# Optimization experiments

Measured on AMD Instinct MI355X. Metric: run time of the kernel, lower is better.

Reference implementation:

```python
import jax, jax.numpy as jnp
import numpy as np

N = 50000      # nodes
E = 640000     # edges
HID = 64       # hid_dim (per-head channels C)
HEADS = 4
D = HID * HEADS  # 256, conv output dim (concat=True)
LN_EPS = 1e-5


def setup_inputs() -> dict:
    key = jax.random.key(0)
    ks = jax.random.split(key, 10)
    def w(k, shape, scale=0.05):
        return jax.random.normal(k, shape, dtype=jnp.float32) * scale
    x = jax.random.normal(ks[0], (N, HID), dtype=jnp.float32)
    edge_index = jax.random.randint(ks[1], (2, E), 0, N)
    return {
        'x': x,
        'edge_index': edge_index,
        'Wq': w(ks[2], (D, HID)), 'bq': jnp.zeros((D,), jnp.float32),
        'Wk': w(ks[3], (D, HID)), 'bk': jnp.zeros((D,), jnp.float32),
        'Wv': w(ks[4], (D, HID)), 'bv': jnp.zeros((D,), jnp.float32),
        'Wskip': w(ks[5], (D, HID)), 'bskip': jnp.zeros((D,), jnp.float32),
        'Wbeta': w(ks[6], (1, 3 * D)),
        'ln_g': jnp.ones((D,), jnp.float32), 'ln_b': jnp.zeros((D,), jnp.float32),
        'Wproj': w(ks[7], (HID, D)), 'bproj': jnp.zeros((HID,), jnp.float32),
    }


def _layer(x, edge_index, Wq, bq, Wk, bk, Wv, bv, Wskip, bskip, Wbeta, ln_g, ln_b, Wproj, bproj):
    src, dst = edge_index[0], edge_index[1]  # message flows src -> dst
    # q/k/v projections, [N, H, C]
    q = (x @ Wq.T + bq).reshape(N, HEADS, HID)
    k = (x @ Wk.T + bk).reshape(N, HEADS, HID)
    v = (x @ Wv.T + bv).reshape(N, HEADS, HID)
    # edge-wise attention logits: [E, H]
    alpha = jnp.einsum('ehc,ehc->eh', q[dst], k[src]) / jnp.sqrt(jnp.float32(HID))
    # per-destination-node softmax (segment softmax)
    m = jax.ops.segment_max(alpha, dst, num_segments=N)          # [N, H]
    ex = jnp.exp(alpha - m[dst])                                 # [E, H]
    s = jax.ops.segment_sum(ex, dst, num_segments=N)             # [N, H]
    attn = ex / (s[dst] + 1e-16)                                 # [E, H]
    # weighted scatter-aggregate of values -> [N, H*C]
    msg = (v[src] * attn[..., None]).reshape(E, D)
    out = jax.ops.segment_sum(msg, dst, num_segments=N)          # [N, D]
    # beta gated skip (TransformerConv beta=True, root_weight=True)
    x_r = x @ Wskip.T + bskip                                    # [N, D]
    beta = jax.nn.sigmoid(jnp.concatenate([out, x_r, out - x_r], axis=-1) @ Wbeta.T)  # [N, 1]
    h = beta * x_r + (1.0 - beta) * out
    # LayerNorm over last dim
    mu = jnp.mean(h, axis=-1, keepdims=True)
    var = jnp.var(h, axis=-1, keepdims=True)
    h = (h - mu) * jax.lax.rsqrt(var + LN_EPS) * ln_g + ln_b
    # projection + residual + ReLU (dropout = identity in eval)
    h = h @ Wproj.T + bproj
    return jax.nn.relu(h + x)


def reference(x, edge_index, Wq, bq, Wk, bk, Wv, bv, Wskip, bskip, Wbeta, ln_g, ln_b, Wproj, bproj):
    return _layer(x, edge_index, Wq, bq, Wk, bk, Wv, bv, Wskip, bskip, Wbeta, ln_g, ln_b, Wproj, bproj)
```

## Files before the change

### kernel.cpp

```cpp
#include <hip/hip_runtime.h>
#include <stdint.h>

#define NND 50000
#define NED 640000
#define NCH 196

typedef unsigned short u16;
typedef unsigned int u32;
typedef __attribute__((ext_vector_type(8))) short short8;
typedef __attribute__((ext_vector_type(4))) float f32x4;
typedef __attribute__((ext_vector_type(2))) float fx2;

__device__ __forceinline__ float bf2f(u16 u) {
    union { u32 i; float f; } x; x.i = ((u32)u) << 16; return x.f;
}
__device__ __forceinline__ u16 f2bf(float f) {
    union { u32 i; float f; } x; x.f = f;
    u32 u = x.i;
    return (u16)((u + 0x7fffu + ((u >> 16) & 1u)) >> 16);
}
__device__ __forceinline__ float bflo(u32 w) {
    union { u32 i; float f; } x; x.i = w << 16; return x.f;
}
__device__ __forceinline__ float bfhi(u32 w) {
    union { u32 i; float f; } x; x.i = w & 0xffff0000u; return x.f;
}
__device__ __forceinline__ u32 pk2(float lo, float hi) {
    return (u32)f2bf(lo) | ((u32)f2bf(hi) << 16);
}
__device__ __forceinline__ u32 pk_fp8_4(u32 w0, u32 w1) {
    u32 p = __builtin_amdgcn_cvt_pk_fp8_f32(bflo(w0), bfhi(w0), 0, false);
    p = __builtin_amdgcn_cvt_pk_fp8_f32(bflo(w1), bfhi(w1), p, true);
    return p;
}
__device__ __forceinline__ void dec8(u32 a, u32 b, float* f) {
    fx2 x0 = __builtin_amdgcn_cvt_pk_f32_fp8(a, false);
    fx2 x1 = __builtin_amdgcn_cvt_pk_f32_fp8(a, true);
    fx2 x2 = __builtin_amdgcn_cvt_pk_f32_fp8(b, false);
    fx2 x3 = __builtin_amdgcn_cvt_pk_f32_fp8(b, true);
    f[0] = x0.x; f[1] = x0.y; f[2] = x1.x; f[3] = x1.y;
    f[4] = x2.x; f[5] = x2.y; f[6] = x3.x; f[7] = x3.y;
}

__global__ void k_count(const int* __restrict__ edst, int* __restrict__ deg) {
    int e = blockIdx.x * 256 + threadIdx.x;
    if (e < NED) atomicAdd(&deg[edst[e]], 1);
}

__global__ void k_bsum(const int* __restrict__ deg, int* __restrict__ bsums) {
    int i = blockIdx.x * 256 + threadIdx.x;
    int v = (i < NND) ? deg[i] : 0;
    #pragma unroll
    for (int m = 1; m < 64; m <<= 1) v += __shfl_xor(v, m, 64);
    __shared__ int ls[4];
    if ((threadIdx.x & 63) == 0) ls[threadIdx.x >> 6] = v;
    __syncthreads();
    if (threadIdx.x == 0) bsums[blockIdx.x] = ls[0] + ls[1] + ls[2] + ls[3];
}

__global__ void k_scan(int* __restrict__ bsums) {
    __shared__ int a[256];
    int t = threadIdx.x;
    int v = (t < NCH) ? bsums[t] : 0;
    a[t] = v;
    __syncthreads();
    for (int off = 1; off < 256; off <<= 1) {
        int add = (t >= off) ? a[t - off] : 0;
        __syncthreads();
        a[t] += add;
        __syncthreads();
    }
    if (t < NCH) bsums[t] = a[t] - v;
}

__global__ void k_offsets(const int* __restrict__ deg, const int* __restrict__ bsums,
                          int* __restrict__ offs, int* __restrict__ cursor) {
    __shared__ int a[256];
    int t = threadIdx.x;
    int i = blockIdx.x * 256 + t;
    int v = (i < NND) ? deg[i] : 0;
    a[t] = v;
    __syncthreads();
    for (int off = 1; off < 256; off <<= 1) {
        int add = (t >= off) ? a[t - off] : 0;
        __syncthreads();
        a[t] += add;
        __syncthreads();
    }
    int excl = bsums[blockIdx.x] + a[t] - v;
    if (i < NND) {
        offs[i] = excl;
        cursor[i] = excl;
        if (i == NND - 1) offs[NND] = excl + v;
    }
}

__global__ void k_fill(const int* __restrict__ esrc, const int* __restrict__ edst,
                       int* __restrict__ cursor, int* __restrict__ csr) {
    int e = blockIdx.x * 256 + threadIdx.x;
    if (e < NED) {
        int pos = atomicAdd(&cursor[edst[e]], 1);
        csr[pos] = esrc[e];
    }
}

__global__ void k_wt(const float* __restrict__ Wq, const float* __restrict__ Wk,
                     const float* __restrict__ Wv, const float* __restrict__ Ws,
                     const float* __restrict__ Wp,
                     const float* __restrict__ bq, const float* __restrict__ bk,
                     const float* __restrict__ bv, const float* __restrict__ bs,
                     u16* __restrict__ wb, float* __restrict__ bias_c,
                     u16* __restrict__ wpA, int* __restrict__ deg) {
    int idx = blockIdx.x * 256 + threadIdx.x;
    if (idx < NND) deg[idx] = 0;
    if (idx < 65536) {
        int j = idx & 7;
        int lane = (idx >> 3) & 63;
        int q = (idx >> 9) & 1;
        int dt = idx >> 10;
        int dim = dt * 16 + (lane & 15);
        int k = q * 32 + ((lane >> 4) & 3) * 8 + j;
        int mat = dim >> 8, r = dim & 255;
        const float* W = (mat == 0) ? Wq : (mat == 1) ? Wk : (mat == 2) ? Wv : Ws;
        float v = W[r * 64 + k] * ((mat == 0) ? 0.125f : 1.0f);
        wb[idx] = f2bf(v);
    } else if (idx < 65536 + 1024) {
        int dim = idx - 65536;
        int mat = dim >> 8, r = dim & 255;
        const float* B = (mat == 0) ? bq : (mat == 1) ? bk : (mat == 2) ? bv : bs;
        bias_c[dim] = B[r] * ((mat == 0) ? 0.125f : 1.0f);
    } else if (idx < 65536 + 1024 + 16384) {
        int w = idx - 66560;
        int j = w & 7;
        int lane = (w >> 3) & 63;
        int kc = (w >> 9) & 7;
        int mt = w >> 12;
        int dim = mt * 16 + (lane & 15);
        int k = kc * 32 + ((lane >> 4) & 3) * 8 + j;
        wpA[w] = f2bf(Wp[dim * 256 + k]);
    }
}

#define PPAD 1040
__global__ __launch_bounds__(256) void k_proj(
    const float* __restrict__ x, const u16* __restrict__ wb,
    const float* __restrict__ bias_c,
    uint2* __restrict__ q8, uint4* __restrict__ kv8, u16* __restrict__ xr16)
{
    __shared__ u16 hb[16 * PPAD];
    const int t = threadIdx.x;
    const int wave = t >> 6, lane = t & 63;
    const int nbase = blockIdx.x * 64;
    const int lr = lane & 15, quad = lane >> 4;

    for (int nt = 0; nt < 4; ++nt) {
        const int node0 = nbase + nt * 16;
        if (node0 >= NND) break;
        int node = node0 + lr;
        if (node > NND - 1) node = NND - 1;
        short8 xf0, xf1;
        {
            const float* xp = x + (size_t)node * 64 + quad * 8;
            float4 a = *reinterpret_cast<const float4*>(xp);
            float4 b = *reinterpret_cast<const float4*>(xp + 4);
            float4 c = *reinterpret_cast<const float4*>(xp + 32);
            float4 d = *reinterpret_cast<const float4*>(xp + 36);
            xf0[0] = (short)f2bf(a.x); xf0[1] = (short)f2bf(a.y);
            xf0[2] = (short)f2bf(a.z); xf0[3] = (short)f2bf(a.w);
            xf0[4] = (short)f2bf(b.x); xf0[5] = (short)f2bf(b.y);
            xf0[6] = (short)f2bf(b.z); xf0[7] = (short)f2bf(b.w);
            xf1[0] = (short)f2bf(c.x); xf1[1] = (short)f2bf(c.y);
            xf1[2] = (short)f2bf(c.z); xf1[3] = (short)f2bf(c.w);
            xf1[4] = (short)f2bf(d.x); xf1[5] = (short)f2bf(d.y);
            xf1[6] = (short)f2bf(d.z); xf1[7] = (short)f2bf(d.w);
        }
        #pragma unroll 4
        for (int dtl = 0; dtl < 16; ++dtl) {
            int dt = wave * 16 + dtl;
            const u16* wp = wb + (size_t)(dt * 2) * 512 + lane * 8;
            short8 a0 = *reinterpret_cast<const short8*>(wp);
            short8 a1 = *reinterpret_cast<const short8*>(wp + 512);
            f32x4 bias = *reinterpret_cast<const f32x4*>(bias_c + dt * 16 + quad * 4);
            f32x4 acc = {0.f, 0.f, 0.f, 0.f};
            acc = __builtin_amdgcn_mfma_f32_16x16x32_bf16(a0, xf0, acc, 0, 0, 0);
            acc = __builtin_amdgcn_mfma_f32_16x16x32_bf16(a1, xf1, acc, 0, 0, 0);
            uint2 st;
            st.x = pk2(acc[0] + bias[0], acc[1] + bias[1]);
            st.y = pk2(acc[2] + bias[2], acc[3] + bias[3]);
            *reinterpret_cast<uint2*>(&hb[lr * PPAD + dt * 16 + quad * 4]) = st;
        }
        __syncthreads();
        #pragma unroll
        for (int it = 0; it < 2; ++it) {
            int idx = it * 256 + t;
            int nip = idx >> 5, g = idx & 31;
            int gnode = node0 + nip;
            if (gnode < NND) {
                const u16* hp = &hb[nip * PPAD];
                *reinterpret_cast<uint4*>(xr16 + (size_t)gnode * 256 + g * 8) =
                    *reinterpret_cast<const uint4*>(hp + 768 + g * 8);
                uint4 qw = *reinterpret_cast<const uint4*>(hp + g * 8);
                uint2 qs;
                qs.x = pk_fp8_4(qw.x, qw.y);
                qs.y = pk_fp8_4(qw.z, qw.w);
                q8[(size_t)gnode * 32 + g] = qs;
                uint4 kw = *reinterpret_cast<const uint4*>(hp + 256 + g * 8);
                uint4 vw = *reinterpret_cast<const uint4*>(hp + 512 + g * 8);
                uint4 kvs;
                kvs.x = pk_fp8_4(kw.x, kw.y);
                kvs.y = pk_fp8_4(kw.z, kw.w);
                kvs.z = pk_fp8_4(vw.x, vw.y);
                kvs.w = pk_fp8_4(vw.z, vw.w);
                kv8[(size_t)gnode * 32 + g] = kvs;
            }
        }
        __syncthreads();
    }
}

__global__ __launch_bounds__(256) void k_attn(
    const int* __restrict__ offs, const int* __restrict__ csr,
    const uint2* __restrict__ q8, const uint4* __restrict__ kv8,
    u16* __restrict__ out16)
{
    const int wave = threadIdx.x >> 6;
    const int lane = threadIdx.x & 63;
    const int node = blockIdx.x * 4 + wave;
    if (node >= NND) return;
    const int l32 = lane & 31;
    const int half = lane >> 5;

    uint2 qv = q8[(size_t)node * 32 + l32];
    float q[8];
    dec8(qv.x, qv.y, q);

    int r0 = __builtin_amdgcn_readfirstlane(offs[node]);
    int r1 = __builtin_amdgcn_readfirstlane(offs[node + 1]);

    float s = 0.f;
    float a0 = 0.f, a1 = 0.f, a2 = 0.f, a3 = 0.f;
    float a4 = 0.f, a5 = 0.f, a6 = 0.f, a7 = 0.f;

    int i = r0;
    for (; i + 8 <= r1; i += 8) {
        int c0 = csr[i + 0], c1 = csr[i + 1], c2 = csr[i + 2], c3 = csr[i + 3];
        int c4 = csr[i + 4], c5 = csr[i + 5], c6 = csr[i + 6], c7 = csr[i + 7];
        int e0 = half ? c4 : c0;
        int e1 = half ? c5 : c1;
        int e2 = half ? c6 : c2;
        int e3 = half ? c7 : c3;
        uint4 kv0 = kv8[(size_t)e0 * 32 + l32];
        uint4 kv1 = kv8[(size_t)e1 * 32 + l32];
        uint4 kv2 = kv8[(size_t)e2 * 32 + l32];
        uint4 kv3 = kv8[(size_t)e3 * 32 + l32];
        float k0[8], k1[8], k2[8], k3[8];
        dec8(kv0.x, kv0.y, k0); dec8(kv1.x, kv1.y, k1);
        dec8(kv2.x, kv2.y, k2); dec8(kv3.x, kv3.y, k3);
        float pa = q[0]*k0[0]+q[1]*k0[1]+q[2]*k0[2]+q[3]*k0[3]+q[4]*k0[4]+q[5]*k0[5]+q[6]*k0[6]+q[7]*k0[7];
        float pb = q[0]*k1[0]+q[1]*k1[1]+q[2]*k1[2]+q[3]*k1[3]+q[4]*k1[4]+q[5]*k1[5]+q[6]*k1[6]+q[7]*k1[7];
        float pc = q[0]*k2[0]+q[1]*k2[1]+q[2]*k2[2]+q[3]*k2[3]+q[4]*k2[4]+q[5]*k2[5]+q[6]*k2[6]+q[7]*k2[7];
        float pd = q[0]*k3[0]+q[1]*k3[1]+q[2]*k3[2]+q[3]*k3[3]+q[4]*k3[4]+q[5]*k3[5]+q[6]*k3[6]+q[7]*k3[7];
        pa += __shfl_xor(pa, 1); pa += __shfl_xor(pa, 2); pa += __shfl_xor(pa, 4);
        pb += __shfl_xor(pb, 1); pb += __shfl_xor(pb, 2); pb += __shfl_xor(pb, 4);
        pc += __shfl_xor(pc, 1); pc += __shfl_xor(pc, 2); pc += __shfl_xor(pc, 4);
        pd += __shfl_xor(pd, 1); pd += __shfl_xor(pd, 2); pd += __shfl_xor(pd, 4);
        float ea = __expf(pa), eb = __expf(pb), ec = __expf(pc), ed = __expf(pd);
        s += (ea + eb) + (ec + ed);
        float v0[8], v1[8], v2[8], v3[8];
        dec8(kv0.z, kv0.w, v0); dec8(kv1.z, kv1.w, v1);
        dec8(kv2.z, kv2.w, v2); dec8(kv3.z, kv3.w, v3);
        a0 = fmaf(ea, v0[0], fmaf(eb, v1[0], fmaf(ec, v2[0], fmaf(ed, v3[0], a0))));
        a1 = fmaf(ea, v0[1], fmaf(eb, v1[1], fmaf(ec, v2[1], fmaf(ed, v3[1], a1))));
        a2 = fmaf(ea, v0[2], fmaf(eb, v1[2], fmaf(ec, v2[2], fmaf(ed, v3[2], a2))));
        a3 = fmaf(ea, v0[3], fmaf(eb, v1[3], fmaf(ec, v2[3], fmaf(ed, v3[3], a3))));
        a4 = fmaf(ea, v0[4], fmaf(eb, v1[4], fmaf(ec, v2[4], fmaf(ed, v3[4], a4))));
        a5 = fmaf(ea, v0[5], fmaf(eb, v1[5], fmaf(ec, v2[5], fmaf(ed, v3[5], a5))));
        a6 = fmaf(ea, v0[6], fmaf(eb, v1[6], fmaf(ec, v2[6], fmaf(ed, v3[6], a6))));
        a7 = fmaf(ea, v0[7], fmaf(eb, v1[7], fmaf(ec, v2[7], fmaf(ed, v3[7], a7))));
    }
    for (; i + 4 <= r1; i += 4) {
        int c0 = csr[i + 0], c1 = csr[i + 1], c2 = csr[i + 2], c3 = csr[i + 3];
        int e0 = half ? c2 : c0;
        int e1 = half ? c3 : c1;
        uint4 kv0 = kv8[(size_t)e0 * 32 + l32];
        uint4 kv1 = kv8[(size_t)e1 * 32 + l32];
        float k0[8], k1[8];
        dec8(kv0.x, kv0.y, k0); dec8(kv1.x, kv1.y, k1);
        float pa = q[0]*k0[0]+q[1]*k0[1]+q[2]*k0[2]+q[3]*k0[3]+q[4]*k0[4]+q[5]*k0[5]+q[6]*k0[6]+q[7]*k0[7];
        float pb = q[0]*k1[0]+q[1]*k1[1]+q[2]*k1[2]+q[3]*k1[3]+q[4]*k1[4]+q[5]*k1[5]+q[6]*k1[6]+q[7]*k1[7];
        pa += __shfl_xor(pa, 1); pa += __shfl_xor(pa, 2); pa += __shfl_xor(pa, 4);
        pb += __shfl_xor(pb, 1); pb += __shfl_xor(pb, 2); pb += __shfl_xor(pb, 4);
        float ea = __expf(pa), eb = __expf(pb);
        s += ea + eb;
        float v0[8], v1[8];
        dec8(kv0.z, kv0.w, v0); dec8(kv1.z, kv1.w, v1);
        a0 = fmaf(ea, v0[0], fmaf(eb, v1[0], a0));
        a1 = fmaf(ea, v0[1], fmaf(eb, v1[1], a1));
        a2 = fmaf(ea, v0[2], fmaf(eb, v1[2], a2));
        a3 = fmaf(ea, v0[3], fmaf(eb, v1[3], a3));
        a4 = fmaf(ea, v0[4], fmaf(eb, v1[4], a4));
        a5 = fmaf(ea, v0[5], fmaf(eb, v1[5], a5));
        a6 = fmaf(ea, v0[6], fmaf(eb, v1[6], a6));
        a7 = fmaf(ea, v0[7], fmaf(eb, v1[7], a7));
    }
    for (; i < r1; i += 2) {
        int ii = i + half;
        bool valid = ii < r1;
        if (ii > r1 - 1) ii = r1 - 1;
        int e0 = csr[ii];
        uint4 kv0 = kv8[(size_t)e0 * 32 + l32];
        float k0[8];
        dec8(kv0.x, kv0.y, k0);
        float pa = q[0]*k0[0]+q[1]*k0[1]+q[2]*k0[2]+q[3]*k0[3]+q[4]*k0[4]+q[5]*k0[5]+q[6]*k0[6]+q[7]*k0[7];
        pa += __shfl_xor(pa, 1); pa += __shfl_xor(pa, 2); pa += __shfl_xor(pa, 4);
        float ea = valid ? __expf(pa) : 0.f;
        s += ea;
        float v0[8];
        dec8(kv0.z, kv0.w, v0);
        a0 = fmaf(ea, v0[0], a0);
        a1 = fmaf(ea, v0[1], a1);
        a2 = fmaf(ea, v0[2], a2);
        a3 = fmaf(ea, v0[3], a3);
        a4 = fmaf(ea, v0[4], a4);
        a5 = fmaf(ea, v0[5], a5);
        a6 = fmaf(ea, v0[6], a6);
        a7 = fmaf(ea, v0[7], a7);
    }
    s  += __shfl_xor(s, 32);
    a0 += __shfl_xor(a0, 32); a1 += __shfl_xor(a1, 32);
    a2 += __shfl_xor(a2, 32); a3 += __shfl_xor(a3, 32);
    a4 += __shfl_xor(a4, 32); a5 += __shfl_xor(a5, 32);
    a6 += __shfl_xor(a6, 32); a7 += __shfl_xor(a7, 32);
    float inv = 1.0f / (s + 1e-16f);
    if (half == 0) {
        uint4 st;
        st.x = pk2(a0 * inv, a1 * inv);
        st.y = pk2(a2 * inv, a3 * inv);
        st.z = pk2(a4 * inv, a5 * inv);
        st.w = pk2(a6 * inv, a7 * inv);
        *reinterpret_cast<uint4*>(out16 + (size_t)node * 256 + l32 * 8) = st;
    }
}

#define PS 264
__global__ __launch_bounds__(256) void k_epi(
    const u16* __restrict__ out16, const u16* __restrict__ xr16,
    const float* __restrict__ x, const float* __restrict__ Wbeta,
    const float* __restrict__ ln_g, const float* __restrict__ ln_b,
    const u16* __restrict__ wpA, const float* __restrict__ bproj,
    float* __restrict__ y)
{
    __shared__ u16 hn[64 * PS];
    const int t = threadIdx.x;
    const int wave = t >> 6, lane = t & 63;
    const int lr = lane & 15;
    const int grp = lane >> 4;
    const int base = blockIdx.x * 64;

    const float4* wb4 = reinterpret_cast<const float4*>(Wbeta);
    const float4* g44 = reinterpret_cast<const float4*>(ln_g);
    const float4* b44 = reinterpret_cast<const float4*>(ln_b);
    float wo[16], wx[16], wd[16], gg[16], bb[16];
    #pragma unroll
    for (int j = 0; j < 4; ++j) {
        float4 a = wb4[lr * 4 + j];
        float4 b = wb4[64 + lr * 4 + j];
        float4 c = wb4[128 + lr * 4 + j];
        float4 g = g44[lr * 4 + j];
        float4 bl = b44[lr * 4 + j];
        wo[j*4+0]=a.x; wo[j*4+1]=a.y; wo[j*4+2]=a.z; wo[j*4+3]=a.w;
        wx[j*4+0]=b.x; wx[j*4+1]=b.y; wx[j*4+2]=b.z; wx[j*4+3]=b.w;
        wd[j*4+0]=c.x; wd[j*4+1]=c.y; wd[j*4+2]=c.z; wd[j*4+3]=c.w;
        gg[j*4+0]=g.x; gg[j*4+1]=g.y; gg[j*4+2]=g.z; gg[j*4+3]=g.w;
        bb[j*4+0]=bl.x; bb[j*4+1]=bl.y; bb[j*4+2]=bl.z; bb[j*4+3]=bl.w;
    }

    #pragma unroll
    for (int it = 0; it < 4; ++it) {
        int lid = wave * 16 + it * 4 + grp;
        int node = base + lid;
        if (node < NND) {
            const uint4* op = reinterpret_cast<const uint4*>(out16 + (size_t)node * 256 + lr * 16);
            const uint4* xp = reinterpret_cast<const uint4*>(xr16 + (size_t)node * 256 + lr * 16);
            uint4 u0 = op[0], u1 = op[1];
            uint4 v0 = xp[0], v1 = xp[1];
            float o[16], r[16];
            o[0]=bflo(u0.x); o[1]=bfhi(u0.x); o[2]=bflo(u0.y); o[3]=bfhi(u0.y);
            o[4]=bflo(u0.z); o[5]=bfhi(u0.z); o[6]=bflo(u0.w); o[7]=bfhi(u0.w);
            o[8]=bflo(u1.x); o[9]=bfhi(u1.x); o[10]=bflo(u1.y); o[11]=bfhi(u1.y);
            o[12]=bflo(u1.z); o[13]=bfhi(u1.z); o[14]=bflo(u1.w); o[15]=bfhi(u1.w);
            r[0]=bflo(v0.x); r[1]=bfhi(v0.x); r[2]=bflo(v0.y); r[3]=bfhi(v0.y);
            r[4]=bflo(v0.z); r[5]=bfhi(v0.z); r[6]=bflo(v0.w); r[7]=bfhi(v0.w);
            r[8]=bflo(v1.x); r[9]=bfhi(v1.x); r[10]=bflo(v1.y); r[11]=bfhi(v1.y);
            r[12]=bflo(v1.z); r[13]=bfhi(v1.z); r[14]=bflo(v1.w); r[15]=bfhi(v1.w);
            float part = 0.f;
            #pragma unroll
            for (int cc = 0; cc < 16; ++cc)
                part = fmaf(wo[cc], o[cc], fmaf(wx[cc], r[cc], fmaf(wd[cc], o[cc]-r[cc], part)));
            part += __shfl_xor(part, 1); part += __shfl_xor(part, 2);
            part += __shfl_xor(part, 4); part += __shfl_xor(part, 8);
            float beta = 1.0f / (1.0f + __expf(-part));
            float h[16];
            float sh = 0.f, sq = 0.f;
            #pragma unroll
            for (int cc = 0; cc < 16; ++cc) {
                h[cc] = beta * r[cc] + (1.f - beta) * o[cc];
                sh += h[cc];
                sq = fmaf(h[cc], h[cc], sq);
            }
            sh += __shfl_xor(sh, 1); sh += __shfl_xor(sh, 2);
            sh += __shfl_xor(sh, 4); sh += __shfl_xor(sh, 8);
            sq += __shfl_xor(sq, 1); sq += __shfl_xor(sq, 2);
            sq += __shfl_xor(sq, 4); sq += __shfl_xor(sq, 8);
            float mu = sh * (1.0f / 256.0f);
            float var = sq * (1.0f / 256.0f) - mu * mu;
            float ri = rsqrtf(var + 1e-5f);
            u32 pw[8];
            #pragma unroll
            for (int p = 0; p < 8; ++p) {
                float z0 = (h[p*2+0] - mu) * ri * gg[p*2+0] + bb[p*2+0];
                float z1 = (h[p*2+1] - mu) * ri * gg[p*2+1] + bb[p*2+1];
                pw[p] = pk2(z0, z1);
            }
            uint4 s0, s1;
            s0.x = pw[0]; s0.y = pw[1]; s0.z = pw[2]; s0.w = pw[3];
            s1.x = pw[4]; s1.y = pw[5]; s1.z = pw[6]; s1.w = pw[7];
            *reinterpret_cast<uint4*>(&hn[lid * PS + lr * 16]) = s0;
            *reinterpret_cast<uint4*>(&hn[lid * PS + lr * 16 + 8]) = s1;
        }
    }
    __syncthreads();

    const int node = base + wave * 16 + lr;
    #pragma unroll
    for (int mt = 0; mt < 4; ++mt) {
        f32x4 acc = {0.f, 0.f, 0.f, 0.f};
        #pragma unroll
        for (int kc = 0; kc < 8; ++kc) {
            short8 a = *reinterpret_cast<const short8*>(wpA + ((size_t)(mt * 8 + kc) * 64 + lane) * 8);
            short8 b = *reinterpret_cast<const short8*>(&hn[(wave * 16 + lr) * PS + kc * 32 + grp * 8]);
            acc = __builtin_amdgcn_mfma_f32_16x16x32_bf16(a, b, acc, 0, 0, 0);
        }
        if (node < NND) {
            int d0 = mt * 16 + grp * 4;
            float4 bp4 = *reinterpret_cast<const float4*>(bproj + d0);
            float4 xv = *reinterpret_cast<const float4*>(x + (size_t)node * 64 + d0);
            float4 rr;
            rr.x = fmaxf(acc[0] + bp4.x + xv.x, 0.f);
            rr.y = fmaxf(acc[1] + bp4.y + xv.y, 0.f);
            rr.z = fmaxf(acc[2] + bp4.z + xv.z, 0.f);
            rr.w = fmaxf(acc[3] + bp4.w + xv.w, 0.f);
            *reinterpret_cast<float4*>(y + (size_t)node * 64 + d0) = rr;
        }
    }
}

extern "C" void kernel_launch(void* const* d_in, const int* in_sizes, int n_in,
                              void* d_out, int out_size, void* d_ws, size_t ws_size,
                              hipStream_t stream) {
    const float* x     = (const float*)d_in[0];
    const int*   eidx  = (const int*)d_in[1];
    const float* Wq    = (const float*)d_in[2];
    const float* bq    = (const float*)d_in[3];
    const float* Wk    = (const float*)d_in[4];
    const float* bk    = (const float*)d_in[5];
    const float* Wv    = (const float*)d_in[6];
    const float* bv    = (const float*)d_in[7];
    const float* Wsk   = (const float*)d_in[8];
    const float* bsk   = (const float*)d_in[9];
    const float* Wbeta = (const float*)d_in[10];
    const float* lng   = (const float*)d_in[11];
    const float* lnb   = (const float*)d_in[12];
    const float* Wp    = (const float*)d_in[13];
    const float* bp    = (const float*)d_in[14];
    float* y = (float*)d_out;

    char* ws = (char*)d_ws;
    size_t off = 0;
    auto alloc = [&](size_t b) { size_t o = off; off += (b + 255) & ~(size_t)255; return o; };
    uint2* q8   = (uint2*)(ws + alloc((size_t)NND * 256));
    uint4* kv8  = (uint4*)(ws + alloc((size_t)NND * 512));
    u16*  xr16  = (u16*)(ws + alloc((size_t)NND * 512));
    u16*  out16 = (u16*)(ws + alloc((size_t)NND * 512));
    int* deg    = (int*)(ws + alloc((size_t)NND * 4));
    int* offs   = (int*)(ws + alloc((size_t)(NND + 1) * 4));
    int* cursor = (int*)(ws + alloc((size_t)NND * 4));
    int* csr    = (int*)(ws + alloc((size_t)NED * 4));
    int* bsums  = (int*)(ws + alloc((size_t)NCH * 4));
    u16* wb     = (u16*)(ws + alloc((size_t)65536 * 2));
    float* bias_c = (float*)(ws + alloc((size_t)1024 * 4));
    u16* wpA    = (u16*)(ws + alloc((size_t)16384 * 2));

    k_wt     <<<(66560 + 16384 + 255) / 256, 256, 0, stream>>>(
                 Wq, Wk, Wv, Wsk, Wp, bq, bk, bv, bsk, wb, bias_c, wpA, deg);
    k_count  <<<(NED + 255) / 256, 256, 0, stream>>>(eidx + NED, deg);
    k_bsum   <<<NCH, 256, 0, stream>>>(deg, bsums);
    k_scan   <<<1, 256, 0, stream>>>(bsums);
    k_offsets<<<NCH, 256, 0, stream>>>(deg, bsums, offs, cursor);
    k_fill   <<<(NED + 255) / 256, 256, 0, stream>>>(eidx, eidx + NED, cursor, csr);
    k_proj   <<<(NND + 63) / 64, 256, 0, stream>>>(x, wb, bias_c, q8, kv8, xr16);
    k_attn   <<<(NND + 3) / 4, 256, 0, stream>>>(offs, csr, q8, kv8, out16);
    k_epi    <<<(NND + 63) / 64, 256, 0, stream>>>(out16, xr16, x, Wbeta, lng, lnb, wpA, bp, y);
}
```

Measured before the change: 268.3 us.

## Recompute skip projection in epilogue and use packed float2 math in attention

The skip projection x_r is no longer computed in k_proj and stored to global memory as bf16. k_epi now recomputes it with MFMA from x into shared memory, which removes a 25.6 MB write and read round trip at the cost of extra MFMA work and shared-memory pressure in the epilogue. The attention kernel's fp8 decode, dot products and value accumulation are also rewritten with float2 vectors so the compiler can emit packed FMA instructions. The k_proj shared buffer shrinks because only q, k and v are staged.

```diff
diff --git a/kernel.cpp b/kernel.cpp
--- a/kernel.cpp
+++ b/kernel.cpp
@@ -33,13 +33,11 @@
     p = __builtin_amdgcn_cvt_pk_fp8_f32(bflo(w1), bfhi(w1), p, true);
     return p;
 }
-__device__ __forceinline__ void dec8(u32 a, u32 b, float* f) {
-    fx2 x0 = __builtin_amdgcn_cvt_pk_f32_fp8(a, false);
-    fx2 x1 = __builtin_amdgcn_cvt_pk_f32_fp8(a, true);
-    fx2 x2 = __builtin_amdgcn_cvt_pk_f32_fp8(b, false);
-    fx2 x3 = __builtin_amdgcn_cvt_pk_f32_fp8(b, true);
-    f[0] = x0.x; f[1] = x0.y; f[2] = x1.x; f[3] = x1.y;
-    f[4] = x2.x; f[5] = x2.y; f[6] = x3.x; f[7] = x3.y;
+__device__ __forceinline__ void dec8v(u32 a, u32 b, fx2* f) {
+    f[0] = __builtin_amdgcn_cvt_pk_f32_fp8(a, false);
+    f[1] = __builtin_amdgcn_cvt_pk_f32_fp8(a, true);
+    f[2] = __builtin_amdgcn_cvt_pk_f32_fp8(b, false);
+    f[3] = __builtin_amdgcn_cvt_pk_f32_fp8(b, true);
 }
 
 __global__ void k_count(const int* __restrict__ edst, int* __restrict__ deg) {
@@ -141,11 +139,11 @@
     }
 }
 
-#define PPAD 1040
+#define PPAD 784
 __global__ __launch_bounds__(256) void k_proj(
     const float* __restrict__ x, const u16* __restrict__ wb,
     const float* __restrict__ bias_c,
-    uint2* __restrict__ q8, uint4* __restrict__ kv8, u16* __restrict__ xr16)
+    uint2* __restrict__ q8, uint4* __restrict__ kv8)
 {
     __shared__ u16 hb[16 * PPAD];
     const int t = threadIdx.x;
@@ -175,8 +173,8 @@
             xf1[6] = (short)f2bf(d.z); xf1[7] = (short)f2bf(d.w);
         }
         #pragma unroll 4
-        for (int dtl = 0; dtl < 16; ++dtl) {
-            int dt = wave * 16 + dtl;
+        for (int dtl = 0; dtl < 12; ++dtl) {
+            int dt = wave * 12 + dtl;
             const u16* wp = wb + (size_t)(dt * 2) * 512 + lane * 8;
             short8 a0 = *reinterpret_cast<const short8*>(wp);
             short8 a1 = *reinterpret_cast<const short8*>(wp + 512);
@@ -197,8 +195,6 @@
             int gnode = node0 + nip;
             if (gnode < NND) {
                 const u16* hp = &hb[nip * PPAD];
-                *reinterpret_cast<uint4*>(xr16 + (size_t)gnode * 256 + g * 8) =
-                    *reinterpret_cast<const uint4*>(hp + 768 + g * 8);
                 uint4 qw = *reinterpret_cast<const uint4*>(hp + g * 8);
                 uint2 qs;
                 qs.x = pk_fp8_4(qw.x, qw.y);
@@ -231,15 +227,14 @@
     const int half = lane >> 5;
 
     uint2 qv = q8[(size_t)node * 32 + l32];
-    float q[8];
-    dec8(qv.x, qv.y, q);
+    fx2 q[4];
+    dec8v(qv.x, qv.y, q);
 
     int r0 = __builtin_amdgcn_readfirstlane(offs[node]);
     int r1 = __builtin_amdgcn_readfirstlane(offs[node + 1]);
 
     float s = 0.f;
-    float a0 = 0.f, a1 = 0.f, a2 = 0.f, a3 = 0.f;
-    float a4 = 0.f, a5 = 0.f, a6 = 0.f, a7 = 0.f;
+    fx2 acc0 = {0.f, 0.f}, acc1 = {0.f, 0.f}, acc2 = {0.f, 0.f}, acc3 = {0.f, 0.f};
 
     int i = r0;
     for (; i + 8 <= r1; i += 8) {
@@ -253,30 +248,28 @@
         uint4 kv1 = kv8[(size_t)e1 * 32 + l32];
         uint4 kv2 = kv8[(size_t)e2 * 32 + l32];
         uint4 kv3 = kv8[(size_t)e3 * 32 + l32];
-        float k0[8], k1[8], k2[8], k3[8];
-        dec8(kv0.x, kv0.y, k0); dec8(kv1.x, kv1.y, k1);
-        dec8(kv2.x, kv2.y, k2); dec8(kv3.x, kv3.y, k3);
-        float pa = q[0]*k0[0]+q[1]*k0[1]+q[2]*k0[2]+q[3]*k0[3]+q[4]*k0[4]+q[5]*k0[5]+q[6]*k0[6]+q[7]*k0[7];
-        float pb = q[0]*k1[0]+q[1]*k1[1]+q[2]*k1[2]+q[3]*k1[3]+q[4]*k1[4]+q[5]*k1[5]+q[6]*k1[6]+q[7]*k1[7];
-        float pc = q[0]*k2[0]+q[1]*k2[1]+q[2]*k2[2]+q[3]*k2[3]+q[4]*k2[4]+q[5]*k2[5]+q[6]*k2[6]+q[7]*k2[7];
-        float pd = q[0]*k3[0]+q[1]*k3[1]+q[2]*k3[2]+q[3]*k3[3]+q[4]*k3[4]+q[5]*k3[5]+q[6]*k3[6]+q[7]*k3[7];
+        fx2 k0[4], k1[4], k2[4], k3[4];
+        dec8v(kv0.x, kv0.y, k0); dec8v(kv1.x, kv1.y, k1);
+        dec8v(kv2.x, kv2.y, k2); dec8v(kv3.x, kv3.y, k3);
+        fx2 t0 = q[0]*k0[0] + q[1]*k0[1] + q[2]*k0[2] + q[3]*k0[3];
+        fx2 t1 = q[0]*k1[0] + q[1]*k1[1] + q[2]*k1[2] + q[3]*k1[3];
+        fx2 t2 = q[0]*k2[0] + q[1]*k2[1] + q[2]*k2[2] + q[3]*k2[3];
+        fx2 t3 = q[0]*k3[0] + q[1]*k3[1] + q[2]*k3[2] + q[3]*k3[3];
+        float pa = t0.x + t0.y, pb = t1.x + t1.y, pc = t2.x + t2.y, pd = t3.x + t3.y;
         pa += __shfl_xor(pa, 1); pa += __shfl_xor(pa, 2); pa += __shfl_xor(pa, 4);
         pb += __shfl_xor(pb, 1); pb += __shfl_xor(pb, 2); pb += __shfl_xor(pb, 4);
         pc += __shfl_xor(pc, 1); pc += __shfl_xor(pc, 2); pc += __shfl_xor(pc, 4);
         pd += __shfl_xor(pd, 1); pd += __shfl_xor(pd, 2); pd += __shfl_xor(pd, 4);
         float ea = __expf(pa), eb = __expf(pb), ec = __expf(pc), ed = __expf(pd);
         s += (ea + eb) + (ec + ed);
-        float v0[8], v1[8], v2[8], v3[8];
-        dec8(kv0.z, kv0.w, v0); dec8(kv1.z, kv1.w, v1);
-        dec8(kv2.z, kv2.w, v2); dec8(kv3.z, kv3.w, v3);
-        a0 = fmaf(ea, v0[0], fmaf(eb, v1[0], fmaf(ec, v2[0], fmaf(ed, v3[0], a0))));
-        a1 = fmaf(ea, v0[1], fmaf(eb, v1[1], fmaf(ec, v2[1], fmaf(ed, v3[1], a1))));
-        a2 = fmaf(ea, v0[2], fmaf(eb, v1[2], fmaf(ec, v2[2], fmaf(ed, v3[2], a2))));
-        a3 = fmaf(ea, v0[3], fmaf(eb, v1[3], fmaf(ec, v2[3], fmaf(ed, v3[3], a3))));
-        a4 = fmaf(ea, v0[4], fmaf(eb, v1[4], fmaf(ec, v2[4], fmaf(ed, v3[4], a4))));
-        a5 = fmaf(ea, v0[5], fmaf(eb, v1[5], fmaf(ec, v2[5], fmaf(ed, v3[5], a5))));
-        a6 = fmaf(ea, v0[6], fmaf(eb, v1[6], fmaf(ec, v2[6], fmaf(ed, v3[6], a6))));
-        a7 = fmaf(ea, v0[7], fmaf(eb, v1[7], fmaf(ec, v2[7], fmaf(ed, v3[7], a7))));
+        fx2 ev0 = {ea, ea}, ev1 = {eb, eb}, ev2 = {ec, ec}, ev3 = {ed, ed};
+        fx2 v0[4], v1[4], v2[4], v3[4];
+        dec8v(kv0.z, kv0.w, v0); dec8v(kv1.z, kv1.w, v1);
+        dec8v(kv2.z, kv2.w, v2); dec8v(kv3.z, kv3.w, v3);
+        acc0 = acc0 + ev0*v0[0] + ev1*v1[0] + ev2*v2[0] + ev3*v3[0];
+        acc1 = acc1 + ev0*v0[1] + ev1*v1[1] + ev2*v2[1] + ev3*v3[1];
+        acc2 = acc2 + ev0*v0[2] + ev1*v1[2] + ev2*v2[2] + ev3*v3[2];
+        acc3 = acc3 + ev0*v0[3] + ev1*v1[3] + ev2*v2[3] + ev3*v3[3];
     }
     for (; i + 4 <= r1; i += 4) {
         int c0 = csr[i + 0], c1 = csr[i + 1], c2 = csr[i + 2], c3 = csr[i + 3];
@@ -284,24 +277,22 @@
         int e1 = half ? c3 : c1;
         uint4 kv0 = kv8[(size_t)e0 * 32 + l32];
         uint4 kv1 = kv8[(size_t)e1 * 32 + l32];
-        float k0[8], k1[8];
-        dec8(kv0.x, kv0.y, k0); dec8(kv1.x, kv1.y, k1);
-        float pa = q[0]*k0[0]+q[1]*k0[1]+q[2]*k0[2]+q[3]*k0[3]+q[4]*k0[4]+q[5]*k0[5]+q[6]*k0[6]+q[7]*k0[7];
-        float pb = q[0]*k1[0]+q[1]*k1[1]+q[2]*k1[2]+q[3]*k1[3]+q[4]*k1[4]+q[5]*k1[5]+q[6]*k1[6]+q[7]*k1[7];
+        fx2 k0[4], k1[4];
+        dec8v(kv0.x, kv0.y, k0); dec8v(kv1.x, kv1.y, k1);
+        fx2 t0 = q[0]*k0[0] + q[1]*k0[1] + q[2]*k0[2] + q[3]*k0[3];
+        fx2 t1 = q[0]*k1[0] + q[1]*k1[1] + q[2]*k1[2] + q[3]*k1[3];
+        float pa = t0.x + t0.y, pb = t1.x + t1.y;
         pa += __shfl_xor(pa, 1); pa += __shfl_xor(pa, 2); pa += __shfl_xor(pa, 4);
         pb += __shfl_xor(pb, 1); pb += __shfl_xor(pb, 2); pb += __shfl_xor(pb, 4);
         float ea = __expf(pa), eb = __expf(pb);
         s += ea + eb;
-        float v0[8], v1[8];
-        dec8(kv0.z, kv0.w, v0); dec8(kv1.z, kv1.w, v1);
-        a0 = fmaf(ea, v0[0], fmaf(eb, v1[0], a0));
-        a1 = fmaf(ea, v0[1], fmaf(eb, v1[1], a1));
-        a2 = fmaf(ea, v0[2], fmaf(eb, v1[2], a2));
-        a3 = fmaf(ea, v0[3], fmaf(eb, v1[3], a3));
-        a4 = fmaf(ea, v0[4], fmaf(eb, v1[4], a4));
-        a5 = fmaf(ea, v0[5], fmaf(eb, v1[5], a5));
-        a6 = fmaf(ea, v0[6], fmaf(eb, v1[6], a6));
-        a7 = fmaf(ea, v0[7], fmaf(eb, v1[7], a7));
+        fx2 ev0 = {ea, ea}, ev1 = {eb, eb};
+        fx2 v0[4], v1[4];
+        dec8v(kv0.z, kv0.w, v0); dec8v(kv1.z, kv1.w, v1);
+        acc0 = acc0 + ev0*v0[0] + ev1*v1[0];
+        acc1 = acc1 + ev0*v0[1] + ev1*v1[1];
+        acc2 = acc2 + ev0*v0[2] + ev1*v1[2];
+        acc3 = acc3 + ev0*v0[3] + ev1*v1[3];
     }
     for (; i < r1; i += 2) {
         int ii = i + half;
@@ -309,23 +300,23 @@
         if (ii > r1 - 1) ii = r1 - 1;
         int e0 = csr[ii];
         uint4 kv0 = kv8[(size_t)e0 * 32 + l32];
-        float k0[8];
-        dec8(kv0.x, kv0.y, k0);
-        float pa = q[0]*k0[0]+q[1]*k0[1]+q[2]*k0[2]+q[3]*k0[3]+q[4]*k0[4]+q[5]*k0[5]+q[6]*k0[6]+q[7]*k0[7];
+        fx2 k0[4];
+        dec8v(kv0.x, kv0.y, k0);
+        fx2 t0 = q[0]*k0[0] + q[1]*k0[1] + q[2]*k0[2] + q[3]*k0[3];
+        float pa = t0.x + t0.y;
         pa += __shfl_xor(pa, 1); pa += __shfl_xor(pa, 2); pa += __shfl_xor(pa, 4);
         float ea = valid ? __expf(pa) : 0.f;
         s += ea;
-        float v0[8];
-        dec8(kv0.z, kv0.w, v0);
-        a0 = fmaf(ea, v0[0], a0);
-        a1 = fmaf(ea, v0[1], a1);
-        a2 = fmaf(ea, v0[2], a2);
-        a3 = fmaf(ea, v0[3], a3);
-        a4 = fmaf(ea, v0[4], a4);
-        a5 = fmaf(ea, v0[5], a5);
-        a6 = fmaf(ea, v0[6], a6);
-        a7 = fmaf(ea, v0[7], a7);
-    }
+        fx2 ev0 = {ea, ea};
+        fx2 v0[4];
+        dec8v(kv0.z, kv0.w, v0);
+        acc0 = acc0 + ev0*v0[0];
+        acc1 = acc1 + ev0*v0[1];
+        acc2 = acc2 + ev0*v0[2];
+        acc3 = acc3 + ev0*v0[3];
+    }
+    float a0 = acc0.x, a1 = acc0.y, a2 = acc1.x, a3 = acc1.y;
+    float a4 = acc2.x, a5 = acc2.y, a6 = acc3.x, a7 = acc3.y;
     s  += __shfl_xor(s, 32);
     a0 += __shfl_xor(a0, 32); a1 += __shfl_xor(a1, 32);
     a2 += __shfl_xor(a2, 32); a3 += __shfl_xor(a3, 32);
@@ -344,11 +335,11 @@
 
 #define PS 264
 __global__ __launch_bounds__(256) void k_epi(
-    const u16* __restrict__ out16, const u16* __restrict__ xr16,
-    const float* __restrict__ x, const float* __restrict__ Wbeta,
-    const float* __restrict__ ln_g, const float* __restrict__ ln_b,
-    const u16* __restrict__ wpA, const float* __restrict__ bproj,
-    float* __restrict__ y)
+    const u16* __restrict__ out16, const float* __restrict__ x,
+    const float* __restrict__ Wbeta, const float* __restrict__ ln_g,
+    const float* __restrict__ ln_b, const u16* __restrict__ wb,
+    const float* __restrict__ bias_c, const u16* __restrict__ wpA,
+    const float* __restrict__ bproj, float* __restrict__ y)
 {
     __shared__ u16 hn[64 * PS];
     const int t = threadIdx.x;
@@ -356,6 +347,41 @@
     const int lr = lane & 15;
     const int grp = lane >> 4;
     const int base = blockIdx.x * 64;
+
+    {
+        int node = base + wave * 16 + lr;
+        if (node > NND - 1) node = NND - 1;
+        short8 xf0, xf1;
+        const float* xp = x + (size_t)node * 64 + grp * 8;
+        float4 a = *reinterpret_cast<const float4*>(xp);
+        float4 b = *reinterpret_cast<const float4*>(xp + 4);
+        float4 c = *reinterpret_cast<const float4*>(xp + 32);
+        float4 d = *reinterpret_cast<const float4*>(xp + 36);
+        xf0[0] = (short)f2bf(a.x); xf0[1] = (short)f2bf(a.y);
+        xf0[2] = (short)f2bf(a.z); xf0[3] = (short)f2bf(a.w);
+        xf0[4] = (short)f2bf(b.x); xf0[5] = (short)f2bf(b.y);
+        xf0[6] = (short)f2bf(b.z); xf0[7] = (short)f2bf(b.w);
+        xf1[0] = (short)f2bf(c.x); xf1[1] = (short)f2bf(c.y);
+        xf1[2] = (short)f2bf(c.z); xf1[3] = (short)f2bf(c.w);
+        xf1[4] = (short)f2bf(d.x); xf1[5] = (short)f2bf(d.y);
+        xf1[6] = (short)f2bf(d.z); xf1[7] = (short)f2bf(d.w);
+        #pragma unroll 4
+        for (int mt = 0; mt < 16; ++mt) {
+            int dt = 48 + mt;
+            const u16* wp = wb + (size_t)(dt * 2) * 512 + lane * 8;
+            short8 a0 = *reinterpret_cast<const short8*>(wp);
+            short8 a1 = *reinterpret_cast<const short8*>(wp + 512);
+            f32x4 bias = *reinterpret_cast<const f32x4*>(bias_c + dt * 16 + grp * 4);
+            f32x4 acc = {0.f, 0.f, 0.f, 0.f};
+            acc = __builtin_amdgcn_mfma_f32_16x16x32_bf16(a0, xf0, acc, 0, 0, 0);
+            acc = __builtin_amdgcn_mfma_f32_16x16x32_bf16(a1, xf1, acc, 0, 0, 0);
+            uint2 st;
+            st.x = pk2(acc[0] + bias[0], acc[1] + bias[1]);
+            st.y = pk2(acc[2] + bias[2], acc[3] + bias[3]);
+            *reinterpret_cast<uint2*>(&hn[(wave * 16 + lr) * PS + mt * 16 + grp * 4]) = st;
+        }
+    }
+    __syncthreads();
 
     const float4* wb4 = reinterpret_cast<const float4*>(Wbeta);
     const float4* g44 = reinterpret_cast<const float4*>(ln_g);
@@ -374,16 +400,15 @@
         gg[j*4+0]=g.x; gg[j*4+1]=g.y; gg[j*4+2]=g.z; gg[j*4+3]=g.w;
         bb[j*4+0]=bl.x; bb[j*4+1]=bl.y; bb[j*4+2]=bl.z; bb[j*4+3]=bl.w;
     }
-
     #pragma unroll
     for (int it = 0; it < 4; ++it) {
         int lid = wave * 16 + it * 4 + grp;
         int node = base + lid;
         if (node < NND) {
             const uint4* op = reinterpret_cast<const uint4*>(out16 + (size_t)node * 256 + lr * 16);
-            const uint4* xp = reinterpret_cast<const uint4*>(xr16 + (size_t)node * 256 + lr * 16);
             uint4 u0 = op[0], u1 = op[1];
-            uint4 v0 = xp[0], v1 = xp[1];
+            uint4 v0 = *reinterpret_cast<const uint4*>(&hn[lid * PS + lr * 16]);
+            uint4 v1 = *reinterpret_cast<const uint4*>(&hn[lid * PS + lr * 16 + 8]);
             float o[16], r[16];
             o[0]=bflo(u0.x); o[1]=bfhi(u0.x); o[2]=bflo(u0.y); o[3]=bfhi(u0.y);
             o[4]=bflo(u0.z); o[5]=bfhi(u0.z); o[6]=bflo(u0.w); o[7]=bfhi(u0.w);
@@ -480,7 +505,6 @@
     auto alloc = [&](size_t b) { size_t o = off; off += (b + 255) & ~(size_t)255; return o; };
     uint2* q8   = (uint2*)(ws + alloc((size_t)NND * 256));
     uint4* kv8  = (uint4*)(ws + alloc((size_t)NND * 512));
-    u16*  xr16  = (u16*)(ws + alloc((size_t)NND * 512));
     u16*  out16 = (u16*)(ws + alloc((size_t)NND * 512));
     int* deg    = (int*)(ws + alloc((size_t)NND * 4));
     int* offs   = (int*)(ws + alloc((size_t)(NND + 1) * 4));
@@ -498,7 +522,8 @@
     k_scan   <<<1, 256, 0, stream>>>(bsums);
     k_offsets<<<NCH, 256, 0, stream>>>(deg, bsums, offs, cursor);
     k_fill   <<<(NED + 255) / 256, 256, 0, stream>>>(eidx, eidx + NED, cursor, csr);
-    k_proj   <<<(NND + 63) / 64, 256, 0, stream>>>(x, wb, bias_c, q8, kv8, xr16);
+    k_proj   <<<(NND + 63) / 64, 256, 0, stream>>>(x, wb, bias_c, q8, kv8);
     k_attn   <<<(NND + 3) / 4, 256, 0, stream>>>(offs, csr, q8, kv8, out16);
-    k_epi    <<<(NND + 63) / 64, 256, 0, stream>>>(out16, xr16, x, Wbeta, lng, lnb, wpA, bp, y);
-}
+    k_epi    <<<(NND + 63) / 64, 256, 0, stream>>>(out16, x, Wbeta, lng, lnb,
+                                                   wb, bias_c, wpA, bp, y);
+}
```

New measurement: 275.6 us. 1.03x slower.

## Pad CSR rows to multiples of eight and use packed fx2 math in attention

Applied to the files above, without the earlier changes.

Each node's CSR row is rounded up to a multiple of 8, and the padding slots are filled with node 0. The attention kernel can then run a single 8-edge loop, masking padded edges by setting their exp weight to zero, in place of the earlier 8/4/2 tail loops. Dot products and value accumulation now use float2 vectors, which may map to packed FMA instructions. This removes tail-loop divergence and extra code, at the cost of wasted gathers on padded slots (about 3.5 extra per node on average) and a larger CSR buffer.

```diff
diff --git a/kernel.cpp b/kernel.cpp
--- a/kernel.cpp
+++ b/kernel.cpp
@@ -33,13 +33,11 @@
     p = __builtin_amdgcn_cvt_pk_fp8_f32(bflo(w1), bfhi(w1), p, true);
     return p;
 }
-__device__ __forceinline__ void dec8(u32 a, u32 b, float* f) {
-    fx2 x0 = __builtin_amdgcn_cvt_pk_f32_fp8(a, false);
-    fx2 x1 = __builtin_amdgcn_cvt_pk_f32_fp8(a, true);
-    fx2 x2 = __builtin_amdgcn_cvt_pk_f32_fp8(b, false);
-    fx2 x3 = __builtin_amdgcn_cvt_pk_f32_fp8(b, true);
-    f[0] = x0.x; f[1] = x0.y; f[2] = x1.x; f[3] = x1.y;
-    f[4] = x2.x; f[5] = x2.y; f[6] = x3.x; f[7] = x3.y;
+__device__ __forceinline__ void dec8v(u32 a, u32 b, fx2* f) {
+    f[0] = __builtin_amdgcn_cvt_pk_f32_fp8(a, false);
+    f[1] = __builtin_amdgcn_cvt_pk_f32_fp8(a, true);
+    f[2] = __builtin_amdgcn_cvt_pk_f32_fp8(b, false);
+    f[3] = __builtin_amdgcn_cvt_pk_f32_fp8(b, true);
 }
 
 __global__ void k_count(const int* __restrict__ edst, int* __restrict__ deg) {
@@ -49,7 +47,7 @@
 
 __global__ void k_bsum(const int* __restrict__ deg, int* __restrict__ bsums) {
     int i = blockIdx.x * 256 + threadIdx.x;
-    int v = (i < NND) ? deg[i] : 0;
+    int v = (i < NND) ? ((deg[i] + 7) & ~7) : 0;
     #pragma unroll
     for (int m = 1; m < 64; m <<= 1) v += __shfl_xor(v, m, 64);
     __shared__ int ls[4];
@@ -74,12 +72,14 @@
 }
 
 __global__ void k_offsets(const int* __restrict__ deg, const int* __restrict__ bsums,
-                          int* __restrict__ offs, int* __restrict__ cursor) {
+                          int* __restrict__ offs, int* __restrict__ cursor,
+                          int* __restrict__ csr) {
     __shared__ int a[256];
     int t = threadIdx.x;
     int i = blockIdx.x * 256 + t;
-    int v = (i < NND) ? deg[i] : 0;
-    a[t] = v;
+    int d = (i < NND) ? deg[i] : 0;
+    int cap = (d + 7) & ~7;
+    a[t] = cap;
     __syncthreads();
     for (int off = 1; off < 256; off <<= 1) {
         int add = (t >= off) ? a[t - off] : 0;
@@ -87,11 +87,11 @@
         a[t] += add;
         __syncthreads();
     }
-    int excl = bsums[blockIdx.x] + a[t] - v;
+    int excl = bsums[blockIdx.x] + a[t] - cap;
     if (i < NND) {
         offs[i] = excl;
         cursor[i] = excl;
-        if (i == NND - 1) offs[NND] = excl + v;
+        for (int j = d; j < cap; ++j) csr[excl + j] = 0;
     }
 }
 
@@ -219,7 +219,8 @@
 }
 
 __global__ __launch_bounds__(256) void k_attn(
-    const int* __restrict__ offs, const int* __restrict__ csr,
+    const int* __restrict__ offs, const int* __restrict__ deg,
+    const int* __restrict__ csr,
     const uint2* __restrict__ q8, const uint4* __restrict__ kv8,
     u16* __restrict__ out16)
 {
@@ -231,18 +232,18 @@
     const int half = lane >> 5;
 
     uint2 qv = q8[(size_t)node * 32 + l32];
-    float q[8];
-    dec8(qv.x, qv.y, q);
+    fx2 q[4];
+    dec8v(qv.x, qv.y, q);
 
     int r0 = __builtin_amdgcn_readfirstlane(offs[node]);
-    int r1 = __builtin_amdgcn_readfirstlane(offs[node + 1]);
+    int dg = __builtin_amdgcn_readfirstlane(deg[node]);
+    int cap = (dg + 7) & ~7;
 
     float s = 0.f;
-    float a0 = 0.f, a1 = 0.f, a2 = 0.f, a3 = 0.f;
-    float a4 = 0.f, a5 = 0.f, a6 = 0.f, a7 = 0.f;
-
-    int i = r0;
-    for (; i + 8 <= r1; i += 8) {
+    fx2 acc0 = {0.f, 0.f}, acc1 = {0.f, 0.f}, acc2 = {0.f, 0.f}, acc3 = {0.f, 0.f};
+
+    for (int rel = 0; rel < cap; rel += 8) {
+        int i = r0 + rel;
         int c0 = csr[i + 0], c1 = csr[i + 1], c2 = csr[i + 2], c3 = csr[i + 3];
         int c4 = csr[i + 4], c5 = csr[i + 5], c6 = csr[i + 6], c7 = csr[i + 7];
         int e0 = half ? c4 : c0;
@@ -253,79 +254,35 @@
         uint4 kv1 = kv8[(size_t)e1 * 32 + l32];
         uint4 kv2 = kv8[(size_t)e2 * 32 + l32];
         uint4 kv3 = kv8[(size_t)e3 * 32 + l32];
-        float k0[8], k1[8], k2[8], k3[8];
-        dec8(kv0.x, kv0.y, k0); dec8(kv1.x, kv1.y, k1);
-        dec8(kv2.x, kv2.y, k2); dec8(kv3.x, kv3.y, k3);
-        float pa = q[0]*k0[0]+q[1]*k0[1]+q[2]*k0[2]+q[3]*k0[3]+q[4]*k0[4]+q[5]*k0[5]+q[6]*k0[6]+q[7]*k0[7];
-        float pb = q[0]*k1[0]+q[1]*k1[1]+q[2]*k1[2]+q[3]*k1[3]+q[4]*k1[4]+q[5]*k1[5]+q[6]*k1[6]+q[7]*k1[7];
-        float pc = q[0]*k2[0]+q[1]*k2[1]+q[2]*k2[2]+q[3]*k2[3]+q[4]*k2[4]+q[5]*k2[5]+q[6]*k2[6]+q[7]*k2[7];
-        float pd = q[0]*k3[0]+q[1]*k3[1]+q[2]*k3[2]+q[3]*k3[3]+q[4]*k3[4]+q[5]*k3[5]+q[6]*k3[6]+q[7]*k3[7];
+        fx2 k0[4], k1[4], k2[4], k3[4];
+        dec8v(kv0.x, kv0.y, k0); dec8v(kv1.x, kv1.y, k1);
+        dec8v(kv2.x, kv2.y, k2); dec8v(kv3.x, kv3.y, k3);
+        fx2 t0 = q[0]*k0[0] + q[1]*k0[1] + q[2]*k0[2] + q[3]*k0[3];
+        fx2 t1 = q[0]*k1[0] + q[1]*k1[1] + q[2]*k1[2] + q[3]*k1[3];
+        fx2 t2 = q[0]*k2[0] + q[1]*k2[1] + q[2]*k2[2] + q[3]*k2[3];
+        fx2 t3 = q[0]*k3[0] + q[1]*k3[1] + q[2]*k3[2] + q[3]*k3[3];
+        float pa = t0.x + t0.y, pb = t1.x + t1.y, pc = t2.x + t2.y, pd = t3.x + t3.y;
         pa += __shfl_xor(pa, 1); pa += __shfl_xor(pa, 2); pa += __shfl_xor(pa, 4);
         pb += __shfl_xor(pb, 1); pb += __shfl_xor(pb, 2); pb += __shfl_xor(pb, 4);
         pc += __shfl_xor(pc, 1); pc += __shfl_xor(pc, 2); pc += __shfl_xor(pc, 4);
         pd += __shfl_xor(pd, 1); pd += __shfl_xor(pd, 2); pd += __shfl_xor(pd, 4);
-        float ea = __expf(pa), eb = __expf(pb), ec = __expf(pc), ed = __expf(pd);
+        int rb = rel + half * 4;
+        float ea = (rb + 0 < dg) ? __expf(pa) : 0.f;
+        float eb = (rb + 1 < dg) ? __expf(pb) : 0.f;
+        float ec = (rb + 2 < dg) ? __expf(pc) : 0.f;
+        float ed = (rb + 3 < dg) ? __expf(pd) : 0.f;
         s += (ea + eb) + (ec + ed);
-        float v0[8], v1[8], v2[8], v3[8];
-        dec8(kv0.z, kv0.w, v0); dec8(kv1.z, kv1.w, v1);
-        dec8(kv2.z, kv2.w, v2); dec8(kv3.z, kv3.w, v3);
-        a0 = fmaf(ea, v0[0], fmaf(eb, v1[0], fmaf(ec, v2[0], fmaf(ed, v3[0], a0))));
-        a1 = fmaf(ea, v0[1], fmaf(eb, v1[1], fmaf(ec, v2[1], fmaf(ed, v3[1], a1))));
-        a2 = fmaf(ea, v0[2], fmaf(eb, v1[2], fmaf(ec, v2[2], fmaf(ed, v3[2], a2))));
-        a3 = fmaf(ea, v0[3], fmaf(eb, v1[3], fmaf(ec, v2[3], fmaf(ed, v3[3], a3))));
-        a4 = fmaf(ea, v0[4], fmaf(eb, v1[4], fmaf(ec, v2[4], fmaf(ed, v3[4], a4))));
-        a5 = fmaf(ea, v0[5], fmaf(eb, v1[5], fmaf(ec, v2[5], fmaf(ed, v3[5], a5))));
-        a6 = fmaf(ea, v0[6], fmaf(eb, v1[6], fmaf(ec, v2[6], fmaf(ed, v3[6], a6))));
-        a7 = fmaf(ea, v0[7], fmaf(eb, v1[7], fmaf(ec, v2[7], fmaf(ed, v3[7], a7))));
-    }
-    for (; i + 4 <= r1; i += 4) {
-        int c0 = csr[i + 0], c1 = csr[i + 1], c2 = csr[i + 2], c3 = csr[i + 3];
-        int e0 = half ? c2 : c0;
-        int e1 = half ? c3 : c1;
-        uint4 kv0 = kv8[(size_t)e0 * 32 + l32];
-        uint4 kv1 = kv8[(size_t)e1 * 32 + l32];
-        float k0[8], k1[8];
-        dec8(kv0.x, kv0.y, k0); dec8(kv1.x, kv1.y, k1);
-        float pa = q[0]*k0[0]+q[1]*k0[1]+q[2]*k0[2]+q[3]*k0[3]+q[4]*k0[4]+q[5]*k0[5]+q[6]*k0[6]+q[7]*k0[7];
-        float pb = q[0]*k1[0]+q[1]*k1[1]+q[2]*k1[2]+q[3]*k1[3]+q[4]*k1[4]+q[5]*k1[5]+q[6]*k1[6]+q[7]*k1[7];
-        pa += __shfl_xor(pa, 1); pa += __shfl_xor(pa, 2); pa += __shfl_xor(pa, 4);
-        pb += __shfl_xor(pb, 1); pb += __shfl_xor(pb, 2); pb += __shfl_xor(pb, 4);
-        float ea = __expf(pa), eb = __expf(pb);
-        s += ea + eb;
-        float v0[8], v1[8];
-        dec8(kv0.z, kv0.w, v0); dec8(kv1.z, kv1.w, v1);
-        a0 = fmaf(ea, v0[0], fmaf(eb, v1[0], a0));
-        a1 = fmaf(ea, v0[1], fmaf(eb, v1[1], a1));
-        a2 = fmaf(ea, v0[2], fmaf(eb, v1[2], a2));
-        a3 = fmaf(ea, v0[3], fmaf(eb, v1[3], a3));
-        a4 = fmaf(ea, v0[4], fmaf(eb, v1[4], a4));
-        a5 = fmaf(ea, v0[5], fmaf(eb, v1[5], a5));
-        a6 = fmaf(ea, v0[6], fmaf(eb, v1[6], a6));
-        a7 = fmaf(ea, v0[7], fmaf(eb, v1[7], a7));
-    }
-    for (; i < r1; i += 2) {
-        int ii = i + half;
-        bool valid = ii < r1;
-        if (ii > r1 - 1) ii = r1 - 1;
-        int e0 = csr[ii];
-        uint4 kv0 = kv8[(size_t)e0 * 32 + l32];
-        float k0[8];
-        dec8(kv0.x, kv0.y, k0);
-        float pa = q[0]*k0[0]+q[1]*k0[1]+q[2]*k0[2]+q[3]*k0[3]+q[4]*k0[4]+q[5]*k0[5]+q[6]*k0[6]+q[7]*k0[7];
-        pa += __shfl_xor(pa, 1); pa += __shfl_xor(pa, 2); pa += __shfl_xor(pa, 4);
-        float ea = valid ? __expf(pa) : 0.f;
-        s += ea;
-        float v0[8];
-        dec8(kv0.z, kv0.w, v0);
-        a0 = fmaf(ea, v0[0], a0);
-        a1 = fmaf(ea, v0[1], a1);
-        a2 = fmaf(ea, v0[2], a2);
-        a3 = fmaf(ea, v0[3], a3);
-        a4 = fmaf(ea, v0[4], a4);
-        a5 = fmaf(ea, v0[5], a5);
-        a6 = fmaf(ea, v0[6], a6);
-        a7 = fmaf(ea, v0[7], a7);
-    }
+        fx2 ev0 = {ea, ea}, ev1 = {eb, eb}, ev2 = {ec, ec}, ev3 = {ed, ed};
+        fx2 v0[4], v1[4], v2[4], v3[4];
+        dec8v(kv0.z, kv0.w, v0); dec8v(kv1.z, kv1.w, v1);
+        dec8v(kv2.z, kv2.w, v2); dec8v(kv3.z, kv3.w, v3);
+        acc0 = acc0 + ev0*v0[0] + ev1*v1[0] + ev2*v2[0] + ev3*v3[0];
+        acc1 = acc1 + ev0*v0[1] + ev1*v1[1] + ev2*v2[1] + ev3*v3[1];
+        acc2 = acc2 + ev0*v0[2] + ev1*v1[2] + ev2*v2[2] + ev3*v3[2];
+        acc3 = acc3 + ev0*v0[3] + ev1*v1[3] + ev2*v2[3] + ev3*v3[3];
+    }
+    float a0 = acc0.x, a1 = acc0.y, a2 = acc1.x, a3 = acc1.y;
+    float a4 = acc2.x, a5 = acc2.y, a6 = acc3.x, a7 = acc3.y;
     s  += __shfl_xor(s, 32);
     a0 += __shfl_xor(a0, 32); a1 += __shfl_xor(a1, 32);
     a2 += __shfl_xor(a2, 32); a3 += __shfl_xor(a3, 32);
@@ -485,7 +442,7 @@
     int* deg    = (int*)(ws + alloc((size_t)NND * 4));
     int* offs   = (int*)(ws + alloc((size_t)(NND + 1) * 4));
     int* cursor = (int*)(ws + alloc((size_t)NND * 4));
-    int* csr    = (int*)(ws + alloc((size_t)NED * 4));
+    int* csr    = (int*)(ws + alloc((size_t)(NED + NND * 8) * 4));
     int* bsums  = (int*)(ws + alloc((size_t)NCH * 4));
     u16* wb     = (u16*)(ws + alloc((size_t)65536 * 2));
     float* bias_c = (float*)(ws + alloc((size_t)1024 * 4));
@@ -496,9 +453,10 @@
     k_count  <<<(NED + 255) / 256, 256, 0, stream>>>(eidx + NED, deg);
     k_bsum   <<<NCH, 256, 0, stream>>>(deg, bsums);
     k_scan   <<<1, 256, 0, stream>>>(bsums);
-    k_offsets<<<NCH, 256, 0, stream>>>(deg, bsums, offs, cursor);
+    k_offsets<<<NCH, 256, 0, stream>>>(deg, bsums, offs, cursor, csr);
     k_fill   <<<(NED + 255) / 256, 256, 0, stream>>>(eidx, eidx + NED, cursor, csr);
     k_proj   <<<(NND + 63) / 64, 256, 0, stream>>>(x, wb, bias_c, q8, kv8, xr16);
-    k_attn   <<<(NND + 3) / 4, 256, 0, stream>>>(offs, csr, q8, kv8, out16);
-    k_epi    <<<(NND + 63) / 64, 256, 0, stream>>>(out16, xr16, x, Wbeta, lng, lnb, wpA, bp, y);
-}
+    k_attn   <<<(NND + 3) / 4, 256, 0, stream>>>(offs, deg, csr, q8, kv8, out16);
+    k_epi    <<<(NND + 63) / 64, 256, 0, stream>>>(out16, xr16, x, Wbeta, lng, lnb,
+                                                   wpA, bp, y);
+}
```

Result: slower. 274.4 us (+2.3%).
